# Kernel tuning notes

Hardware: AMD Instinct MI355X
Metric: run time of the kernel (lower is better)

Reference implementation:

```python
import jax, jax.numpy as jnp
import numpy as np

ALPHA = 1.0


def setup_inputs() -> dict:
    key = jax.random.key(0)
    k1, k2 = jax.random.split(key)
    N, D, K = 262144, 256, 256
    x = jax.random.normal(k1, (N, D), dtype=jnp.float32)
    clusters = jax.random.normal(k2, (K, D), dtype=jnp.float32)
    return {"x": x, "clusters": clusters}


def reference(x, clusters):
    # Squared euclidean distance to each cluster center without materializing
    x_sq = jnp.sum(x * x, axis=1, keepdims=True)            # (N, 1)
    c_sq = jnp.sum(clusters * clusters, axis=1)[None, :]    # (1, K)
    cross = jnp.einsum('nd,kd->nk', x, clusters)            # (N, K)
    sq_dist = x_sq - 2.0 * cross + c_sq                     # (N, K)
    # Student-t kernel (as in t-SNE / DEC): q_ij = (1 + d^2/alpha)^(-(alpha+1)/2)
    q = 1.0 / (1.0 + sq_dist / ALPHA)
    q = q ** ((ALPHA + 1.0) / 2.0)
    # Row-normalize to soft assignment probabilities.
    q = q / jnp.sum(q, axis=1, keepdims=True)
    return q
```

## Files before the change

### kernel.cpp

```cpp
#include <hip/hip_runtime.h>


#define NROWS 262144
#define DDIM  256
#define KCL   256
#define TPB   16
#define GRID  (NROWS / 64 / TPB)

using f32x4  = __attribute__((ext_vector_type(4))) float;
using s16x8  = __attribute__((ext_vector_type(8))) short;

__device__ inline unsigned short f2bf(float f) {
    unsigned int u = __float_as_uint(f);
    u += 0x7fffu + ((u >> 16) & 1u);
    return (unsigned short)(u >> 16);
}

__global__ void prep_kernel(const float* __restrict__ clusters,
                            unsigned short* __restrict__ cb,
                            float* __restrict__ csq) {
    int k    = blockIdx.x;
    int lane = threadIdx.x;
    const float* row = clusters + (size_t)k * DDIM;
    float4 a = *reinterpret_cast<const float4*>(row + lane * 4);
    ushort4 b;
    b.x = f2bf(a.x); b.y = f2bf(a.y); b.z = f2bf(a.z); b.w = f2bf(a.w);
    *reinterpret_cast<ushort4*>(cb + (size_t)k * DDIM + lane * 4) = b;
    float ss = a.x*a.x + a.y*a.y + a.z*a.z + a.w*a.w;
    #pragma unroll
    for (int m = 1; m < 64; m <<= 1) ss += __shfl_xor(ss, m);
    if (lane == 0) csq[k] = ss;
}

__global__ __launch_bounds__(512, 2) void fused_kernel(
    const float* __restrict__ x,
    const unsigned short* __restrict__ cb,
    const float* __restrict__ csq,
    float* __restrict__ out) {

    __shared__ char  lds_b[KCL * DDIM * 2];
    __shared__ float ls_sum[TPB][2][4][16];
    __shared__ int   ls_flag[2][4];

    const int tid  = threadIdx.x;
    const int lane = tid & 63;
    const int wave = tid >> 6;
    const int rg   = wave >> 1;
    const int ch   = wave & 1;
    const int c15  = lane & 15;
    const int kch  = lane >> 4;

    const int tile0 = blockIdx.x * TPB;

    #pragma unroll
    for (int it = 0; it < 16; ++it) {
        int slot = it * 8192 + tid * 16;
        int src  = slot ^ (((slot >> 9) & 7) << 4);
        __builtin_amdgcn_global_load_lds(
            (const __attribute__((address_space(1))) unsigned int*)((const char*)cb + src),
            (__attribute__((address_space(3))) unsigned int*)(lds_b + slot),
            16, 0, 0);
    }

    if (tid < 8) ((int*)ls_flag)[tid] = 0;

    float cs[8];
    #pragma unroll
    for (int f = 0; f < 8; ++f) cs[f] = csq[ch * 128 + f * 16 + c15];

    __syncthreads();

    auto xrow = [&](int t) -> const float* {
        return x + (size_t)((tile0 + t) * 64 + rg * 16 + c15) * DDIM + kch * 8;
    };

    f32x4 xv1[8], xv2[8];

    {
        const float* xr = xrow(0);
        #pragma unroll
        for (int i = 0; i < 8; ++i)
            xv1[i] = *reinterpret_cast<const f32x4*>(xr + (i >> 1) * 32 + (i & 1) * 4);
    }

    #pragma unroll 1
    for (int t = 0; t < TPB; ++t) {
        const int trow = (tile0 + t) * 64;
        const float* xr = xrow(t);

        s16x8 afrag[8];
        float p[4] = {0.f, 0.f, 0.f, 0.f};

        #pragma unroll
        for (int s4 = 0; s4 < 4; ++s4) {
            f32x4 xa = xv1[2 * s4], xb = xv1[2 * s4 + 1];
            float t0 = xa[0]*xa[0] + xa[1]*xa[1];
            float t1 = xa[2]*xa[2] + xa[3]*xa[3];
            float t2 = xb[0]*xb[0] + xb[1]*xb[1];
            float t3 = xb[2]*xb[2] + xb[3]*xb[3];
            p[s4] += (t0 + t1) + (t2 + t3);
            afrag[s4][0] = (short)f2bf(xa[0]); afrag[s4][1] = (short)f2bf(xa[1]);
            afrag[s4][2] = (short)f2bf(xa[2]); afrag[s4][3] = (short)f2bf(xa[3]);
            afrag[s4][4] = (short)f2bf(xb[0]); afrag[s4][5] = (short)f2bf(xb[1]);
            afrag[s4][6] = (short)f2bf(xb[2]); afrag[s4][7] = (short)f2bf(xb[3]);
        }

        #pragma unroll
        for (int i = 0; i < 8; ++i) {
            int ii = 8 + i;
            xv2[i] = *reinterpret_cast<const f32x4*>(xr + (ii >> 1) * 32 + (ii & 1) * 4);
        }

        f32x4 acc[8];
        #pragma unroll
        for (int f = 0; f < 8; ++f) acc[f] = (f32x4){0.f, 0.f, 0.f, 0.f};

        #pragma unroll
        for (int s = 0; s < 4; ++s) {
            #pragma unroll
            for (int f = 0; f < 8; ++f) {
                int ba = ((ch * 128 + f * 16 + c15) * 512) + s * 64 + kch * 16;
                ba ^= ((c15 & 7) << 4);
                s16x8 bfrag = *reinterpret_cast<const s16x8*>(lds_b + ba);
                acc[f] = __builtin_amdgcn_mfma_f32_16x16x32_bf16(afrag[s], bfrag,
                                                                 acc[f], 0, 0, 0);
            }
        }

        #pragma unroll
        for (int s4 = 0; s4 < 4; ++s4) {
            f32x4 xa = xv2[2 * s4], xb = xv2[2 * s4 + 1];
            float t0 = xa[0]*xa[0] + xa[1]*xa[1];
            float t1 = xa[2]*xa[2] + xa[3]*xa[3];
            float t2 = xb[0]*xb[0] + xb[1]*xb[1];
            float t3 = xb[2]*xb[2] + xb[3]*xb[3];
            p[s4] += (t0 + t1) + (t2 + t3);
            int s = 4 + s4;
            afrag[s][0] = (short)f2bf(xa[0]); afrag[s][1] = (short)f2bf(xa[1]);
            afrag[s][2] = (short)f2bf(xa[2]); afrag[s][3] = (short)f2bf(xa[3]);
            afrag[s][4] = (short)f2bf(xb[0]); afrag[s][5] = (short)f2bf(xb[1]);
            afrag[s][6] = (short)f2bf(xb[2]); afrag[s][7] = (short)f2bf(xb[3]);
        }

        #pragma unroll
        for (int s = 4; s < 8; ++s) {
            #pragma unroll
            for (int f = 0; f < 8; ++f) {
                int ba = ((ch * 128 + f * 16 + c15) * 512) + s * 64 + kch * 16;
                ba ^= ((c15 & 7) << 4);
                s16x8 bfrag = *reinterpret_cast<const s16x8*>(lds_b + ba);
                acc[f] = __builtin_amdgcn_mfma_f32_16x16x32_bf16(afrag[s], bfrag,
                                                                 acc[f], 0, 0, 0);
            }
        }

        if (t + 1 < TPB) {
            const float* xn = xrow(t + 1);
            #pragma unroll
            for (int i = 0; i < 8; ++i)
                xv1[i] = *reinterpret_cast<const f32x4*>(xn + (i >> 1) * 32 + (i & 1) * 4);
        }

        float xsq = (p[0] + p[1]) + (p[2] + p[3]);
        xsq += __shfl_xor(xsq, 16);
        xsq += __shfl_xor(xsq, 32);

        float psum[4];
        #pragma unroll
        for (int r = 0; r < 4; ++r) {
            float xrr = __shfl(xsq, kch * 4 + r);
            float s = 0.f;
            #pragma unroll
            for (int f = 0; f < 8; ++f) {
                float d2 = xrr - 2.0f * acc[f][r] + cs[f];
                float qv = __builtin_amdgcn_rcpf(1.0f + d2);
                acc[f][r] = qv;
                s += qv;
            }
            s += __shfl_xor(s, 1);
            s += __shfl_xor(s, 2);
            s += __shfl_xor(s, 4);
            s += __shfl_xor(s, 8);
            psum[r] = s;
        }

        if (c15 == 0) {
            #pragma unroll
            for (int r = 0; r < 4; ++r)
                ls_sum[t][ch][rg][kch * 4 + r] = psum[r];
        }
        asm volatile("s_waitcnt lgkmcnt(0)" ::: "memory");
        if (lane == 0)
            __atomic_store_n(&ls_flag[ch][rg], t + 1, __ATOMIC_RELAXED);

        volatile int* pf = (volatile int*)&ls_flag[ch ^ 1][rg];
        while (*pf <= t) { }
        asm volatile("" ::: "memory");

        const int row0t = trow + rg * 16;
        #pragma unroll
        for (int r = 0; r < 4; ++r) {
            float other = ls_sum[t][ch ^ 1][rg][kch * 4 + r];
            float inv = __builtin_amdgcn_rcpf(psum[r] + other);
            const size_t orow = (size_t)(row0t + kch * 4 + r) * KCL;
            #pragma unroll
            for (int f = 0; f < 8; ++f) {
                __builtin_nontemporal_store(acc[f][r] * inv,
                                            &out[orow + ch * 128 + f * 16 + c15]);
            }
        }
    }
}

extern "C" void kernel_launch(void* const* d_in, const int* in_sizes, int n_in,
                              void* d_out, int out_size, void* d_ws, size_t ws_size,
                              hipStream_t stream) {
    const float* x        = (const float*)d_in[0];
    const float* clusters = (const float*)d_in[1];
    float* out = (float*)d_out;

    unsigned short* cb  = (unsigned short*)d_ws;
    float*          csq = (float*)((char*)d_ws + (size_t)KCL * DDIM * sizeof(unsigned short));

    prep_kernel<<<KCL, 64, 0, stream>>>(clusters, cb, csq);
    fused_kernel<<<GRID, 512, 0, stream>>>(x, cb, csq, out);
}
```

Before: 131.1 us.

## Switch to persistent 256-block grid with 12 waves and strided strip assignment

Replaces the fixed 256-block grid of 16 tiles each with a persistent-style grid of 256 blocks of 768 threads (6 row-group pairs), where each wave pair processes 16-row strips strided by the total pair count. The partner-sum exchange uses a double-buffered shared slot indexed by strip parity instead of one slot per tile. This raises waves per block so more rows share each LDS copy of the bf16 centroids and spreads any remainder strips evenly across pairs. The intent is better CU occupancy and less per-row cluster-load overhead, but register pressure at 768 threads with 2 blocks per CU may force spills or cut residency to one block.

```diff
diff --git a/kernel.cpp b/kernel.cpp
--- a/kernel.cpp
+++ b/kernel.cpp
@@ -4,8 +4,12 @@
 #define NROWS 262144
 #define DDIM  256
 #define KCL   256
-#define TPB   16
-#define GRID  (NROWS / 64 / TPB)
+#define GRID  256
+#define PPB   6
+#define NPAIRS (GRID * PPB)
+#define NSTRIPS (NROWS / 16)
+#define BASEK (NSTRIPS / NPAIRS)
+#define EXTRA (NSTRIPS % NPAIRS)
 
 using f32x4  = __attribute__((ext_vector_type(4))) float;
 using s16x8  = __attribute__((ext_vector_type(8))) short;
@@ -32,15 +36,15 @@
     if (lane == 0) csq[k] = ss;
 }
 
-__global__ __launch_bounds__(512, 2) void fused_kernel(
+__global__ __launch_bounds__(768, 2) void fused_kernel(
     const float* __restrict__ x,
     const unsigned short* __restrict__ cb,
     const float* __restrict__ csq,
     float* __restrict__ out) {
 
     __shared__ char  lds_b[KCL * DDIM * 2];
-    __shared__ float ls_sum[TPB][2][4][16];
-    __shared__ int   ls_flag[2][4];
+    __shared__ float ls_sum[2][2][PPB][16];
+    __shared__ int   ls_flag[2][PPB];
 
     const int tid  = threadIdx.x;
     const int lane = tid & 63;
@@ -50,19 +54,22 @@
     const int c15  = lane & 15;
     const int kch  = lane >> 4;
 
-    const int tile0 = blockIdx.x * TPB;
-
-    #pragma unroll
-    for (int it = 0; it < 16; ++it) {
-        int slot = it * 8192 + tid * 16;
-        int src  = slot ^ (((slot >> 9) & 7) << 4);
-        __builtin_amdgcn_global_load_lds(
-            (const __attribute__((address_space(1))) unsigned int*)((const char*)cb + src),
-            (__attribute__((address_space(3))) unsigned int*)(lds_b + slot),
-            16, 0, 0);
+    const int g  = blockIdx.x * PPB + rg;
+    const int nk = BASEK + (g < EXTRA ? 1 : 0);
+
+    if (wave < 8) {
+        #pragma unroll
+        for (int it = 0; it < 16; ++it) {
+            int slot = it * 8192 + tid * 16;
+            int src  = slot ^ (((slot >> 9) & 7) << 4);
+            __builtin_amdgcn_global_load_lds(
+                (const __attribute__((address_space(1))) unsigned int*)((const char*)cb + src),
+                (__attribute__((address_space(3))) unsigned int*)(lds_b + slot),
+                16, 0, 0);
+        }
     }
 
-    if (tid < 8) ((int*)ls_flag)[tid] = 0;
+    if (tid < 2 * PPB) ((int*)ls_flag)[tid] = 0;
 
     float cs[8];
     #pragma unroll
@@ -70,8 +77,8 @@
 
     __syncthreads();
 
-    auto xrow = [&](int t) -> const float* {
-        return x + (size_t)((tile0 + t) * 64 + rg * 16 + c15) * DDIM + kch * 8;
+    auto xrow = [&](int k) -> const float* {
+        return x + (size_t)((g + NPAIRS * k) * 16 + c15) * DDIM + kch * 8;
     };
 
     f32x4 xv1[8], xv2[8];
@@ -84,9 +91,9 @@
     }
 
     #pragma unroll 1
-    for (int t = 0; t < TPB; ++t) {
-        const int trow = (tile0 + t) * 64;
-        const float* xr = xrow(t);
+    for (int k = 0; k < nk; ++k) {
+        const int row0t = (g + NPAIRS * k) * 16;
+        const float* xr = xrow(k);
 
         s16x8 afrag[8];
         float p[4] = {0.f, 0.f, 0.f, 0.f};
@@ -154,8 +161,8 @@
             }
         }
 
-        if (t + 1 < TPB) {
-            const float* xn = xrow(t + 1);
+        if (k + 1 < nk) {
+            const float* xn = xrow(k + 1);
             #pragma unroll
             for (int i = 0; i < 8; ++i)
                 xv1[i] = *reinterpret_cast<const f32x4*>(xn + (i >> 1) * 32 + (i & 1) * 4);
@@ -187,20 +194,19 @@
         if (c15 == 0) {
             #pragma unroll
             for (int r = 0; r < 4; ++r)
-                ls_sum[t][ch][rg][kch * 4 + r] = psum[r];
+                ls_sum[k & 1][ch][rg][kch * 4 + r] = psum[r];
         }
         asm volatile("s_waitcnt lgkmcnt(0)" ::: "memory");
         if (lane == 0)
-            __atomic_store_n(&ls_flag[ch][rg], t + 1, __ATOMIC_RELAXED);
+            __atomic_store_n(&ls_flag[ch][rg], k + 1, __ATOMIC_RELAXED);
 
         volatile int* pf = (volatile int*)&ls_flag[ch ^ 1][rg];
-        while (*pf <= t) { }
+        while (*pf <= k) { }
         asm volatile("" ::: "memory");
 
-        const int row0t = trow + rg * 16;
         #pragma unroll
         for (int r = 0; r < 4; ++r) {
-            float other = ls_sum[t][ch ^ 1][rg][kch * 4 + r];
+            float other = ls_sum[k & 1][ch ^ 1][rg][kch * 4 + r];
             float inv = __builtin_amdgcn_rcpf(psum[r] + other);
             const size_t orow = (size_t)(row0t + kch * 4 + r) * KCL;
             #pragma unroll
@@ -223,5 +229,5 @@
     float*          csq = (float*)((char*)d_ws + (size_t)KCL * DDIM * sizeof(unsigned short));
 
     prep_kernel<<<KCL, 64, 0, stream>>>(clusters, cb, csq);
-    fused_kernel<<<GRID, 512, 0, stream>>>(x, cb, csq, out);
-}
+    fused_kernel<<<GRID, 768, 0, stream>>>(x, cb, csq, out);
+}
```

Result: slower. 320.5 us (+144.5%).
